# Performance work log

Measured on AMD Instinct MI355X. Metric: run time of the kernel, lower is better.

The kernel has to match this reference:

```python
import jax, jax.numpy as jnp
import numpy as np

B, C, D = 512, 100000, 512
MARGIN = 0.5  # ArcFace-style additive angular margin


def setup_inputs() -> dict:
    key = jax.random.key(0)
    k1, k2, k3 = jax.random.split(key, 3)
    embeddings = jax.random.normal(k1, (B, D), dtype=jnp.float32)
    labels = jax.random.randint(k2, (B,), 0, C, dtype=jnp.int32)
    weight = 0.01 * jax.random.normal(k3, (C, D), dtype=jnp.float32)  # torch.normal(0, 0.01, (C, D))
    return {"embeddings": embeddings, "labels": labels, "weight": weight}


def _l2_normalize(x, eps=1e-12):
    return x / jnp.maximum(jnp.linalg.norm(x, axis=-1, keepdims=True), eps)


def reference(embeddings, labels, weight):
    cos_m = jnp.cos(MARGIN)
    sin_m = jnp.sin(MARGIN)

    e = _l2_normalize(embeddings)          # (B, D)
    w = _l2_normalize(weight)              # (C, D)
    logits = jnp.clip(jnp.einsum('bd,cd->bc', e, w), -1.0, 1.0)  # (B, C) cosines

    bsz, ncls = logits.shape
    rows = jnp.arange(bsz)
    cos_t = logits[rows, labels]                                   # (B,) cos(theta_y)
    sin_t = jnp.sqrt(jnp.clip(1.0 - cos_t * cos_t, 0.0, None))     # sin(theta_y)
    cos_tm = cos_t * cos_m - sin_t * sin_m                         # cos(theta_y + m)
    sin_tm = sin_t * cos_m + cos_t * sin_m                         # sin(theta_y + m)

    # non-target class indices per row, ascending, skipping the target: (B, C-1)
    base = jnp.arange(ncls - 1)[None, :]
    nt_idx = base + (base >= labels[:, None]).astype(base.dtype)

    # margin_softmax: logits2 = cos(theta_j) - cos(theta_y + m) over non-target j
    nt_logits = jnp.take_along_axis(logits, nt_idx, axis=1)       # (B, C-1)
    logits2 = nt_logits - cos_tm[:, None]

    # no_grad block: weight_m is unit-norm point at angle theta_y+m from e,
    # so ||w_j - w_m||^2 = 2 - 2 <w_j, w_m>  (avoids materializing (B, C, D)).
    w_y = w[labels]                                                # (B, D)
    w_m = (-sin_m * e + sin_tm[:, None] * w_y) / sin_t[:, None]    # (B, D), unit norm
    sim = jnp.einsum('bd,cd->bc', w_m, w)                          # (B, C)
    nt_sim = jnp.take_along_axis(sim, nt_idx, axis=1)              # (B, C-1)
    diff_weight_norm = jax.lax.stop_gradient(
        jnp.sqrt(jnp.clip(2.0 - 2.0 * nt_sim, 0.0, None)))         # (B, C-1)

    e_logits = jnp.sum(jnp.exp(logits2 / diff_weight_norm), axis=1)  # (B,)
    return jnp.mean(jnp.log1p(e_logits))
```

## Files before the change

kernel.cpp:

```cpp
#include <hip/hip_runtime.h>
#include <hip/hip_fp8.h>
#include <math.h>

#define B_SZ 512
#define C_SZ 100000
#define D_SZ 512

#define BM 256
#define BN 128
#define BK 64
#define NTILES 782
#define MT 4
#define NBLK (NTILES * MT)
#define KSTEPS 8
#define DEPTH 3

typedef __attribute__((ext_vector_type(4))) float f32x4;
typedef __attribute__((ext_vector_type(2))) long lx2;

__device__ __forceinline__ void gload_lds16(const void* gptr, void* lptr) {
  __builtin_amdgcn_global_load_lds(
      (const __attribute__((address_space(1))) void*)gptr,
      (__attribute__((address_space(3))) void*)lptr,
      16, 0, 0);
}

__device__ __forceinline__ unsigned char f2fp8(float x) {
  __hip_fp8_e4m3 h(x);
  return (unsigned char)h.__x;
}
__device__ __forceinline__ float fp82f(unsigned int u) {
  __hip_fp8_e4m3 h;
  h.__x = (unsigned char)u;
  return (float)h;
}
__device__ __forceinline__ unsigned int pack4f8(float a, float b, float c, float d) {
  return (unsigned int)f2fp8(a) | ((unsigned int)f2fp8(b) << 8) |
         ((unsigned int)f2fp8(c) << 16) | ((unsigned int)f2fp8(d) << 24);
}

__global__ __launch_bounds__(256) void k_norm_w(const float* __restrict__ w,
                                                unsigned char* __restrict__ w8) {
  const int row = blockIdx.x * 4 + (threadIdx.x >> 6);
  const int lane = threadIdx.x & 63;
  const float4* wr = (const float4*)(w + (size_t)row * D_SZ);
  float4 v0 = wr[lane];
  float4 v1 = wr[64 + lane];
  float ss = v0.x*v0.x + v0.y*v0.y + v0.z*v0.z + v0.w*v0.w
           + v1.x*v1.x + v1.y*v1.y + v1.z*v1.z + v1.w*v1.w;
  #pragma unroll
  for (int o = 32; o; o >>= 1) ss += __shfl_xor(ss, o, 64);
  const float rn = __builtin_amdgcn_rsqf(fmaxf(ss, 1e-24f));
  unsigned int* out = (unsigned int*)(w8 + (size_t)row * D_SZ);
  out[lane] = pack4f8(v0.x * rn, v0.y * rn, v0.z * rn, v0.w * rn);
  out[64 + lane] = pack4f8(v1.x * rn, v1.y * rn, v1.z * rn, v1.w * rn);
}

__global__ __launch_bounds__(64) void k_prep(const float* __restrict__ e,
                                             const int* __restrict__ labels,
                                             const unsigned char* __restrict__ w8,
                                             unsigned char* __restrict__ A8,
                                             float4* __restrict__ params) {
  const int b = blockIdx.x;
  const int lane = threadIdx.x;
  const float4* er = (const float4*)(e + (size_t)b * D_SZ);
  float4 v0 = er[lane], v1 = er[64 + lane];
  float ss = v0.x*v0.x + v0.y*v0.y + v0.z*v0.z + v0.w*v0.w
           + v1.x*v1.x + v1.y*v1.y + v1.z*v1.z + v1.w*v1.w;
  #pragma unroll
  for (int o = 32; o; o >>= 1) ss += __shfl_xor(ss, o, 64);
  const float rn = __builtin_amdgcn_rsqf(fmaxf(ss, 1e-24f));
  v0.x *= rn; v0.y *= rn; v0.z *= rn; v0.w *= rn;
  v1.x *= rn; v1.y *= rn; v1.z *= rn; v1.w *= rn;

  unsigned int* arow_e = (unsigned int*)(A8 + (size_t)(2 * b) * D_SZ);
  arow_e[lane] = pack4f8(v0.x, v0.y, v0.z, v0.w);
  arow_e[64 + lane] = pack4f8(v1.x, v1.y, v1.z, v1.w);

  const int lab = labels[b];
  const unsigned int* wr = (const unsigned int*)(w8 + (size_t)lab * D_SZ);
  unsigned int w0 = wr[lane], w1 = wr[64 + lane];
  unsigned int* arow_w = (unsigned int*)(A8 + (size_t)(2 * b + 1) * D_SZ);
  arow_w[lane] = w0;
  arow_w[64 + lane] = w1;

  float d = v0.x * fp82f(w0 & 255) + v0.y * fp82f((w0 >> 8) & 255)
          + v0.z * fp82f((w0 >> 16) & 255) + v0.w * fp82f(w0 >> 24)
          + v1.x * fp82f(w1 & 255) + v1.y * fp82f((w1 >> 8) & 255)
          + v1.z * fp82f((w1 >> 16) & 255) + v1.w * fp82f(w1 >> 24);
  #pragma unroll
  for (int o = 32; o; o >>= 1) d += __shfl_xor(d, o, 64);

  if (lane == 0) {
    const float cos_m = 0.877582561890372716f;
    const float sin_m = 0.479425538604203000f;
    float cos_t = fminf(fmaxf(d, -1.0f), 1.0f);
    float sin_t = sqrtf(fmaxf(1.0f - cos_t * cos_t, 0.0f));
    float cos_tm = cos_t * cos_m - sin_t * sin_m;
    float sin_tm = sin_t * cos_m + cos_t * sin_m;
    float inv_st = 1.0f / fmaxf(sin_t, 1e-20f);
    params[b] = make_float4(cos_tm, sin_m * inv_st, sin_tm * inv_st, 0.0f);
  }
}

__device__ __forceinline__ float termf(float de, float dwy, float4 p, bool kill) {
  float c = fminf(fmaxf(de, -1.0f), 1.0f);
  float s = p.z * dwy - p.y * de;
  float x = fmaxf(fmaf(-2.0f, s, 2.0f), 1e-20f);
  float t = (c - p.x) * __builtin_amdgcn_rsqf(x);
  float r = __expf(t);
  return kill ? 0.0f : r;
}

__global__ __launch_bounds__(512, 4) void k_gemm(const unsigned char* __restrict__ A8,
                                                 const unsigned char* __restrict__ W8,
                                                 const float4* __restrict__ params,
                                                 const int* __restrict__ labels,
                                                 float* __restrict__ part) {
  __shared__ __align__(16) unsigned char At[DEPTH][BM * BK];
  __shared__ __align__(16) unsigned char Bt[DEPTH][BN * BK];
  __shared__ float ered[128];
  __shared__ float4 pl[128];
  __shared__ int ll[128];

  const int bid = blockIdx.x;
  const int p = (bid & 7) * (NBLK / 8) + (bid >> 3);
  const int nt = p >> 2, mt = p & 3;
  const int t = threadIdx.x;
  const int w = t >> 6, l = t & 63;
  const int m0 = mt * BM;
  const int n0 = nt * BN;
  const int b0 = mt * (BM / 2);

  if (t < 128) {
    ered[t] = 0.0f;
    pl[t] = params[b0 + t];
    ll[t] = labels[b0 + t];
  }

  const int lcA = t & 63;
  const int faA = t >> 6;
  const int aoff0 = (m0 + faA * 16 + (lcA & 15)) * D_SZ + (lcA >> 4) * 16;
  const int aoff1 = (m0 + (8 + faA) * 16 + (lcA & 15)) * D_SZ + (lcA >> 4) * 16;
  int brow = n0 + faA * 16 + (lcA & 15);
  if (brow >= C_SZ) brow = C_SZ - 1;
  const int boff = brow * D_SZ + (lcA >> 4) * 16;

  f32x4 acc[4][4] = {};
  const int wm = (w >> 1) * 64;
  const int wn_ = (w & 1) * 64;
  const int r16 = l & 15;
  const int g = l >> 4;
  const int mfbase = (w >> 1) * 4;
  const int nfbase = (w & 1) * 4;

#define STAGE(d, ts)                                                        \
  do {                                                                      \
    const int k0_ = (ts) * BK;                                              \
    gload_lds16(A8 + aoff0 + k0_, (void*)(At[d] + t * 16));                 \
    gload_lds16(A8 + aoff1 + k0_, (void*)(At[d] + (512 + t) * 16));         \
    gload_lds16(W8 + (size_t)(boff + k0_), (void*)(Bt[d] + t * 16));        \
  } while (0)

  STAGE(0, 0);
  STAGE(1, 1);
  STAGE(2, 2);
  asm volatile("s_waitcnt vmcnt(6) lgkmcnt(0)" ::: "memory");
  __builtin_amdgcn_s_barrier();

  #pragma unroll
  for (int step = 0; step < KSTEPS; ++step) {
    const int d = step % DEPTH;
    lx2 ap[4], bp[4];
    #pragma unroll
    for (int mf = 0; mf < 4; ++mf)
      ap[mf] = *(const lx2*)(At[d] + ((mfbase + mf) * 64 + l) * 16);
    #pragma unroll
    for (int nf = 0; nf < 4; ++nf)
      bp[nf] = *(const lx2*)(Bt[d] + ((nfbase + nf) * 64 + l) * 16);
    #pragma unroll
    for (int mf = 0; mf < 4; ++mf)
      #pragma unroll
      for (int nf = 0; nf < 4; ++nf) {
        acc[mf][nf] = __builtin_amdgcn_mfma_f32_16x16x32_fp8_fp8(
            ap[mf][0], bp[nf][0], acc[mf][nf], 0, 0, 0);
        acc[mf][nf] = __builtin_amdgcn_mfma_f32_16x16x32_fp8_fp8(
            ap[mf][1], bp[nf][1], acc[mf][nf], 0, 0, 0);
      }
    if (step < KSTEPS - 1) {
      asm volatile("s_waitcnt vmcnt(3)" ::: "memory");
      __builtin_amdgcn_s_barrier();
      if (step + DEPTH < KSTEPS)
        STAGE(d, step + DEPTH);
    }
  }
#undef STAGE

  #pragma unroll
  for (int mf = 0; mf < 4; ++mf) {
    int lb = (wm >> 1) + mf * 8 + 2 * g;
    float4 p0 = pl[lb], p1 = pl[lb + 1];
    int lab0 = ll[lb], lab1 = ll[lb + 1];
    float s0 = 0.0f, s1 = 0.0f;
    #pragma unroll
    for (int nf = 0; nf < 4; ++nf) {
      int j = n0 + wn_ + nf * 16 + r16;
      bool oob = (j >= C_SZ);
      f32x4 c = acc[mf][nf];
      s0 += termf(c[0], c[1], p0, oob || (j == lab0));
      s1 += termf(c[2], c[3], p1, oob || (j == lab1));
    }
    #pragma unroll
    for (int o = 1; o < 16; o <<= 1) {
      s0 += __shfl_xor(s0, o, 64);
      s1 += __shfl_xor(s1, o, 64);
    }
    if (r16 == 0) {
      atomicAdd(&ered[lb], s0);
      atomicAdd(&ered[lb + 1], s1);
    }
  }
  __syncthreads();
  if (t < 128) part[(size_t)(b0 + t) * NTILES + nt] = ered[t];
}

__global__ __launch_bounds__(256) void k_rowsum(const float* __restrict__ part,
                                                float* __restrict__ rowsum) {
  const int b = blockIdx.x;
  float s = 0.0f;
  for (int i = threadIdx.x; i < NTILES; i += 256) s += part[(size_t)b * NTILES + i];
  #pragma unroll
  for (int o = 32; o; o >>= 1) s += __shfl_xor(s, o, 64);
  __shared__ float red[4];
  if ((threadIdx.x & 63) == 0) red[threadIdx.x >> 6] = s;
  __syncthreads();
  if (threadIdx.x == 0)
    rowsum[b] = log1pf(red[0] + red[1] + red[2] + red[3]);
}

__global__ __launch_bounds__(512) void k_final(const float* __restrict__ rowsum,
                                               float* __restrict__ out) {
  const int b = threadIdx.x;
  float v = rowsum[b];
  __shared__ float red[512];
  red[b] = v;
  __syncthreads();
  #pragma unroll
  for (int o = 256; o; o >>= 1) {
    if (b < o) red[b] += red[b + o];
    __syncthreads();
  }
  if (b == 0) out[0] = red[0] / (float)B_SZ;
}

extern "C" void kernel_launch(void* const* d_in, const int* in_sizes, int n_in,
                              void* d_out, int out_size, void* d_ws, size_t ws_size,
                              hipStream_t stream) {
  const float* emb = (const float*)d_in[0];
  const int* labels = (const int*)d_in[1];
  const float* w = (const float*)d_in[2];

  char* ws = (char*)d_ws;
  unsigned char* w8 = (unsigned char*)ws;
  size_t off = (size_t)C_SZ * D_SZ;
  unsigned char* A8 = (unsigned char*)(ws + off);
  off += (size_t)2 * B_SZ * D_SZ;
  float4* params = (float4*)(ws + off);
  off += (size_t)B_SZ * 16;
  float* part = (float*)(ws + off);
  off += (size_t)B_SZ * NTILES * 4;
  float* rowsum = (float*)(ws + off);
  off += (size_t)B_SZ * 4;

  k_norm_w<<<dim3(C_SZ / 4), dim3(256), 0, stream>>>(w, w8);
  k_prep<<<dim3(B_SZ), dim3(64), 0, stream>>>(emb, labels, w8, A8, params);
  k_gemm<<<dim3(NBLK), dim3(512), 0, stream>>>(A8, w8, params, labels, part);
  k_rowsum<<<dim3(B_SZ), dim3(256), 0, stream>>>(part, rowsum);
  k_final<<<dim3(1), dim3(512), 0, stream>>>(rowsum, (float*)d_out);
}
```

Baseline: 159.1 us.

## Switch FP8 GEMM to 32x32x64 scaled MFMA with new LDS staging layout

```diff
diff --git a/kernel.cpp b/kernel.cpp
--- a/kernel.cpp
+++ b/kernel.cpp
@@ -16,7 +16,11 @@
 #define DEPTH 3
 
 typedef __attribute__((ext_vector_type(4))) float f32x4;
-typedef __attribute__((ext_vector_type(2))) long lx2;
+typedef __attribute__((ext_vector_type(16))) float f32x16;
+typedef __attribute__((ext_vector_type(4))) int i32x4;
+typedef __attribute__((ext_vector_type(8))) int i32x8;
+
+#define UNITY_SCALE 0x7F7F7F7F
 
 __device__ __forceinline__ void gload_lds16(const void* gptr, void* lptr) {
   __builtin_amdgcn_global_load_lds(
@@ -117,8 +121,8 @@
                                                  const float4* __restrict__ params,
                                                  const int* __restrict__ labels,
                                                  float* __restrict__ part) {
-  __shared__ __align__(16) unsigned char At[DEPTH][BM * BK];
-  __shared__ __align__(16) unsigned char Bt[DEPTH][BN * BK];
+  __shared__ __align__(32) unsigned char At[DEPTH][BM * BK];
+  __shared__ __align__(32) unsigned char Bt[DEPTH][BN * BK];
   __shared__ float ered[128];
   __shared__ float4 pl[128];
   __shared__ int ll[128];
@@ -138,28 +142,25 @@
     ll[t] = labels[b0 + t];
   }
 
-  const int lcA = t & 63;
-  const int faA = t >> 6;
-  const int aoff0 = (m0 + faA * 16 + (lcA & 15)) * D_SZ + (lcA >> 4) * 16;
-  const int aoff1 = (m0 + (8 + faA) * 16 + (lcA & 15)) * D_SZ + (lcA >> 4) * 16;
-  int brow = n0 + faA * 16 + (lcA & 15);
-  if (brow >= C_SZ) brow = C_SZ - 1;
-  const int boff = brow * D_SZ + (lcA >> 4) * 16;
-
-  f32x4 acc[4][4] = {};
-  const int wm = (w >> 1) * 64;
+  const int kpart = ((t >> 5) & 1) * 32 + ((t >> 6) & 1) * 16;
+  const int aoffs0 = (m0 + (t >> 7) * 32 + (t & 31)) * D_SZ + kpart;
+  const int aoffs1 = aoffs0 + 128 * D_SZ;
+  int brow_s = n0 + (t >> 7) * 32 + (t & 31);
+  if (brow_s >= C_SZ) brow_s = C_SZ - 1;
+  const int boffs = brow_s * D_SZ + kpart;
+
+  f32x16 acc[2][2] = {};
   const int wn_ = (w & 1) * 64;
-  const int r16 = l & 15;
-  const int g = l >> 4;
-  const int mfbase = (w >> 1) * 4;
-  const int nfbase = (w & 1) * 4;
+  const int fA = (w >> 1) * 2;
+  const int fB = (w & 1) * 2;
+  const int hi = l >> 5;
 
 #define STAGE(d, ts)                                                        \
   do {                                                                      \
     const int k0_ = (ts) * BK;                                              \
-    gload_lds16(A8 + aoff0 + k0_, (void*)(At[d] + t * 16));                 \
-    gload_lds16(A8 + aoff1 + k0_, (void*)(At[d] + (512 + t) * 16));         \
-    gload_lds16(W8 + (size_t)(boff + k0_), (void*)(Bt[d] + t * 16));        \
+    gload_lds16(A8 + aoffs0 + k0_, (void*)(At[d] + t * 16));                \
+    gload_lds16(A8 + aoffs1 + k0_, (void*)(At[d] + (512 + t) * 16));        \
+    gload_lds16(W8 + (size_t)(boffs + k0_), (void*)(Bt[d] + t * 16));       \
   } while (0)
 
   STAGE(0, 0);
@@ -171,22 +172,28 @@
   #pragma unroll
   for (int step = 0; step < KSTEPS; ++step) {
     const int d = step % DEPTH;
-    lx2 ap[4], bp[4];
-    #pragma unroll
-    for (int mf = 0; mf < 4; ++mf)
-      ap[mf] = *(const lx2*)(At[d] + ((mfbase + mf) * 64 + l) * 16);
-    #pragma unroll
-    for (int nf = 0; nf < 4; ++nf)
-      bp[nf] = *(const lx2*)(Bt[d] + ((nfbase + nf) * 64 + l) * 16);
-    #pragma unroll
-    for (int mf = 0; mf < 4; ++mf)
+    i32x8 av[2], bv[2];
+    #pragma unroll
+    for (int mf = 0; mf < 2; ++mf) {
+      i32x4 lo = *(const i32x4*)(At[d] + (fA + mf) * 2048 + l * 16);
+      i32x4 hig = *(const i32x4*)(At[d] + (fA + mf) * 2048 + 1024 + l * 16);
+      av[mf] = __builtin_shufflevector(lo, hig, 0, 1, 2, 3, 4, 5, 6, 7);
+    }
+    #pragma unroll
+    for (int nf = 0; nf < 2; ++nf) {
+      i32x4 lo = *(const i32x4*)(Bt[d] + (fB + nf) * 2048 + l * 16);
+      i32x4 hig = *(const i32x4*)(Bt[d] + (fB + nf) * 2048 + 1024 + l * 16);
+      bv[nf] = __builtin_shufflevector(lo, hig, 0, 1, 2, 3, 4, 5, 6, 7);
+    }
+    __builtin_amdgcn_s_setprio(1);
+    #pragma unroll
+    for (int mf = 0; mf < 2; ++mf)
       #pragma unroll
-      for (int nf = 0; nf < 4; ++nf) {
-        acc[mf][nf] = __builtin_amdgcn_mfma_f32_16x16x32_fp8_fp8(
-            ap[mf][0], bp[nf][0], acc[mf][nf], 0, 0, 0);
-        acc[mf][nf] = __builtin_amdgcn_mfma_f32_16x16x32_fp8_fp8(
-            ap[mf][1], bp[nf][1], acc[mf][nf], 0, 0, 0);
-      }
+      for (int nf = 0; nf < 2; ++nf)
+        acc[mf][nf] = __builtin_amdgcn_mfma_scale_f32_32x32x64_f8f6f4(
+            av[mf], bv[nf], acc[mf][nf], 0, 0,
+            0, UNITY_SCALE, 0, UNITY_SCALE);
+    __builtin_amdgcn_s_setprio(0);
     if (step < KSTEPS - 1) {
       asm volatile("s_waitcnt vmcnt(3)" ::: "memory");
       __builtin_amdgcn_s_barrier();
@@ -197,27 +204,23 @@
 #undef STAGE
 
   #pragma unroll
-  for (int mf = 0; mf < 4; ++mf) {
-    int lb = (wm >> 1) + mf * 8 + 2 * g;
-    float4 p0 = pl[lb], p1 = pl[lb + 1];
-    int lab0 = ll[lb], lab1 = ll[lb + 1];
-    float s0 = 0.0f, s1 = 0.0f;
-    #pragma unroll
-    for (int nf = 0; nf < 4; ++nf) {
-      int j = n0 + wn_ + nf * 16 + r16;
-      bool oob = (j >= C_SZ);
-      f32x4 c = acc[mf][nf];
-      s0 += termf(c[0], c[1], p0, oob || (j == lab0));
-      s1 += termf(c[2], c[3], p1, oob || (j == lab1));
-    }
-    #pragma unroll
-    for (int o = 1; o < 16; o <<= 1) {
-      s0 += __shfl_xor(s0, o, 64);
-      s1 += __shfl_xor(s1, o, 64);
-    }
-    if (r16 == 0) {
-      atomicAdd(&ered[lb], s0);
-      atomicAdd(&ered[lb + 1], s1);
+  for (int mf = 0; mf < 2; ++mf) {
+    #pragma unroll
+    for (int rp = 0; rp < 8; ++rp) {
+      const int r = 2 * rp;
+      const int lb = (w >> 1) * 32 + mf * 16 + (rp & 1) + 4 * (rp >> 1) + 2 * hi;
+      float4 pp = pl[lb];
+      int lab = ll[lb];
+      float s = 0.0f;
+      #pragma unroll
+      for (int nf = 0; nf < 2; ++nf) {
+        int j = n0 + wn_ + nf * 32 + (l & 31);
+        bool kill = (j >= C_SZ) || (j == lab);
+        s += termf(acc[mf][nf][r], acc[mf][nf][r + 1], pp, kill);
+      }
+      #pragma unroll
+      for (int o = 1; o < 32; o <<= 1) s += __shfl_xor(s, o, 64);
+      if ((l & 31) == 0) atomicAdd(&ered[lb], s);
     }
   }
   __syncthreads();
```

After: 427.2 us. 168% more time.
